# Optimization experiments

Hardware: AMD Instinct MI355X
Metric: run time of the kernel (lower is better)

The kernel has to match this reference:

```python
import jax, jax.numpy as jnp
import numpy as np

K = 16
EPS = 1e-5
SLOPE = 0.01  # nn.LeakyReLU default


def _bn(x, g, b):
    # BatchNorm1d in training mode applied to [N, C, k] in torch == normalize
    # per-channel over (N, k) axes of [N, k, C] here. Biased variance (ddof=0).
    m = x.mean(axis=(0, 1))
    v = x.var(axis=(0, 1))
    return (x - m) * jax.lax.rsqrt(v + EPS) * g + b


def _lrelu(x):
    return jnp.where(x >= 0, x, SLOPE * x)


def setup_inputs() -> dict:
    key = jax.random.key(0)
    ks = jax.random.split(key, 24)
    N, CIN, COUT = 8192, 256, 256
    s = 0.05
    inp = {
        "fea_i": jax.random.normal(ks[0], (N, CIN), jnp.float32),
        "fea_last": jax.random.normal(ks[1], (N, CIN), jnp.float32),
        "xyz_i": jax.random.uniform(ks[2], (N, 3), jnp.float32),
        "xyz_last": jax.random.uniform(ks[3], (N, 3), jnp.float32),
        "t_i": jnp.float32(2.0),
        "t_last": jnp.float32(1.0),
        # lin_p: Linear(4,64) -> BN(64) -> LeakyReLU -> Linear(64,COUT)
        "wp1": jax.random.normal(ks[4], (4, 64), jnp.float32) * s,
        "bp1": jnp.zeros((64,), jnp.float32),
        "gp": jnp.ones((64,), jnp.float32),
        "bp": jnp.zeros((64,), jnp.float32),
        "wp2": jax.random.normal(ks[5], (64, COUT), jnp.float32) * s,
        "bp2": jnp.zeros((COUT,), jnp.float32),
        # lin_q / lin_k / lin_v
        "wq": jax.random.normal(ks[6], (CIN, COUT), jnp.float32) * s,
        "bq": jnp.zeros((COUT,), jnp.float32),
        "wk": jax.random.normal(ks[7], (CIN, COUT), jnp.float32) * s,
        "bk": jnp.zeros((COUT,), jnp.float32),
        "wv": jax.random.normal(ks[8], (CIN, COUT), jnp.float32) * s,
        "bv": jnp.zeros((COUT,), jnp.float32),
        # lin_w: BN -> LeakyReLU -> Linear(COUT,COUT) -> BN -> LeakyReLU
        "gw1": jnp.ones((COUT,), jnp.float32),
        "bw1": jnp.zeros((COUT,), jnp.float32),
        "ww": jax.random.normal(ks[9], (COUT, COUT), jnp.float32) * s,
        "bw": jnp.zeros((COUT,), jnp.float32),
        "gw2": jnp.ones((COUT,), jnp.float32),
        "bw2": jnp.zeros((COUT,), jnp.float32),
    }
    return inp


def reference(fea_i, fea_last, xyz_i, xyz_last, t_i, t_last,
              wp1, bp1, gp, bp, wp2, bp2,
              wq, bq, wk, bk, wv, bv,
              gw1, bw1, ww, bw, gw2, bw2):
    # k-NN: for each query point in xyz_last, K nearest points in xyz_i
    d2 = (jnp.sum(xyz_last * xyz_last, -1)[:, None]
          + jnp.sum(xyz_i * xyz_i, -1)[None, :]
          - 2.0 * xyz_last @ xyz_i.T)              # [N, N]
    idx = jax.lax.top_k(-d2, K)[1]                 # [N, K] neighbor idx into xyz_i

    fi = fea_i[idx]                                # [N, K, CIN]
    xi = xyz_i[idx]                                # [N, K, 3]
    # pe = xyzt_i - xyzt_last ; the gathered "last" side is the query point itself
    pe = jnp.concatenate([xi - xyz_last[:, None, :],
                          (t_i - t_last) * jnp.ones_like(xi[..., :1])], axis=-1)  # [N,K,4]
    pe = pe @ wp1 + bp1
    pe = _lrelu(_bn(pe, gp, bp))
    pe = pe @ wp2 + bp2                            # [N, K, COUT]

    q = fea_last @ wq + bq                         # [N, COUT], broadcast over K
    w = q[:, None, :] - (fi @ wk + bk) + pe        # [N, K, COUT]
    w = _lrelu(_bn(w, gw1, bw1))
    w = w @ ww + bw
    w = _lrelu(_bn(w, gw2, bw2))
    w = jax.nn.softmax(w, axis=1)                  # softmax over K neighbors

    v = fi @ wv + bv + pe                          # [N, K, COUT]
    return jnp.sum(w * v, axis=1)                  # [N, COUT]
```

## Files before the change

kernel.cpp:

```cpp
#include <hip/hip_runtime.h>
#include <hip/hip_bf16.h>
#include <math.h>

#define N     8192
#define KNN   16
#define NK    (N*KNN)
#define C     256
#define CH    64
#define EPS   1e-5f
#define SLOPE 0.01f
#define LISTMAX 512

typedef __hip_bfloat16 bf16;
typedef short bfrag __attribute__((ext_vector_type(8)));
typedef float ffrag __attribute__((ext_vector_type(4)));

__device__ __forceinline__ float b2f(bf16 x){ return __bfloat162float(x); }
__device__ __forceinline__ bf16  f2b(float x){ return __float2bfloat16(x); }
__device__ __forceinline__ float b2fu(unsigned short s){
    return __uint_as_float(((unsigned)s) << 16);
}
__device__ __forceinline__ unsigned short f2bu(float x){
    union { bf16 h; unsigned short s; } u; u.h = f2b(x); return u.s;
}

union BF8 { unsigned short s[8]; uint4 u; };

template<typename T> __device__ __forceinline__ float ldv(const void* p, int i);
template<> __device__ __forceinline__ float ldv<float>(const void* p, int i){
    return ((const float*)p)[i];
}
template<> __device__ __forceinline__ float ldv<bf16>(const void* p, int i){
    return __bfloat162float(((const bf16*)p)[i]);
}
__device__ __forceinline__ bool is_f32(const void* ti){
    return ((const unsigned short*)ti)[0] == 0;
}

template<typename T>
__device__ __forceinline__ void stage8(const void* src, size_t off,
                                       unsigned short* dst){
    if (sizeof(T) == 4){
        const float4* s = (const float4*)((const float*)src + off);
        float4 a = s[0], b = s[1];
        BF8 o;
        o.s[0]=f2bu(a.x); o.s[1]=f2bu(a.y); o.s[2]=f2bu(a.z); o.s[3]=f2bu(a.w);
        o.s[4]=f2bu(b.x); o.s[5]=f2bu(b.y); o.s[6]=f2bu(b.z); o.s[7]=f2bu(b.w);
        *(uint4*)dst = o.u;
    } else {
        *(uint4*)dst = *(const uint4*)((const unsigned short*)src + off);
    }
}

__device__ __forceinline__ int mbcnt64(unsigned long long b){
    return __builtin_amdgcn_mbcnt_hi((unsigned)(b>>32),
           __builtin_amdgcn_mbcnt_lo((unsigned)b, 0));
}
__device__ __forceinline__ unsigned d2key(float d2){
    unsigned u = __float_as_uint(d2);
    return u ^ (((unsigned)(((int)u) >> 31)) | 0x80000000u);
}

__device__ __align__(256) int    g_idx[NK];
__device__ __align__(256) float  g_S[4096];
__device__ __align__(256) float  g_Rep[4*64*256];
__device__ __align__(256) float  g_M2[2048*9];
__device__ __align__(256) float4 g_pts[N];
__device__ __align__(256) int    g_cellCnt[4096];
__device__ __align__(256) int    g_cellStart[4100];
__device__ __align__(256) int    g_cellCur[4096];
__device__ __align__(256) float4 g_spts[N];
__device__ __align__(256) int    g_sidx[N];
__device__ __align__(256) unsigned short g_qT [C*C];
__device__ __align__(256) unsigned short g_kT [C*C];
__device__ __align__(256) unsigned short g_vT [C*C];
__device__ __align__(256) unsigned short g_wwT[C*C];
__device__ __align__(256) unsigned short g_p2T[C*CH];
__device__ __align__(256) unsigned short g_q  [N*C];
__device__ __align__(256) unsigned short g_fkb[N*C];
__device__ __align__(256) unsigned short g_fvb[N*C];
__device__ __align__(256) bf16   g_w1[NK*C];
__device__ __align__(256) bf16   g_vv[NK*C];
__device__ __align__(256) bf16   g_w2[NK*C];

__device__ __forceinline__ int cell_of(float4 c){
    int cx = (int)(c.x*16.f); cx = cx<0?0:(cx>15?15:cx);
    int cy = (int)(c.y*16.f); cy = cy<0?0:(cy>15?15:cy);
    int cz = (int)(c.z*16.f); cz = cz<0?0:(cz>15?15:cz);
    return (cz<<8) | (cy<<4) | cx;
}

__global__ __launch_bounds__(256) void kprepall(const void* xyz_i,
        const void* wq, const void* wk, const void* wv, const void* ww,
        const void* wp2, const void* ti_){
#pragma clang fp contract(off)
    const int b = blockIdx.x, tid = threadIdx.x;
    const bool f = is_f32(ti_);
    if (b < 64){
        int i = b*256 + tid;
        #pragma unroll
        for (int k = 0; k < 4; k++) g_Rep[i*4 + k] = 0.f;
        if (b < 16) g_S[i] = 0.f;
        else if (b < 32) g_cellCnt[(b-16)*256 + tid] = 0;
    } else if (b < 96){
        int p = (b-64)*256 + tid;
        float x = f ? ldv<float>(xyz_i, p*3+0) : ldv<bf16>(xyz_i, p*3+0);
        float y = f ? ldv<float>(xyz_i, p*3+1) : ldv<bf16>(xyz_i, p*3+1);
        float z = f ? ldv<float>(xyz_i, p*3+2) : ldv<bf16>(xyz_i, p*3+2);
        g_pts[p] = make_float4(x, y, z, (x*x + y*y) + z*z);
    } else {
        const void* src; unsigned short* dst; int K; int i0;
        if      (b <  352){ src=wq;  dst=g_qT;  K=256; i0=(b-  96)*256; }
        else if (b <  608){ src=wk;  dst=g_kT;  K=256; i0=(b- 352)*256; }
        else if (b <  864){ src=wv;  dst=g_vT;  K=256; i0=(b- 608)*256; }
        else if (b < 1120){ src=ww;  dst=g_wwT; K=256; i0=(b- 864)*256; }
        else              { src=wp2; dst=g_p2T; K=64;  i0=(b-1120)*256; }
        int i = i0 + tid;
        int k = i >> 8, n = i & 255;
        float v = f ? ldv<float>(src, i) : ldv<bf16>(src, i);
        dst[n*K + k] = f2bu(v);
    }
}

__global__ __launch_bounds__(256) void khist(){
    int p = blockIdx.x*256 + threadIdx.x;
    atomicAdd(&g_cellCnt[cell_of(g_pts[p])], 1);
}
__global__ __launch_bounds__(256) void kscan(){
    __shared__ int sc[256];
    const int tid = threadIdx.x;
    int carry = 0;
    for (int ch = 0; ch < 16; ch++){
        int i = ch*256 + tid;
        int v = g_cellCnt[i];
        sc[tid] = v;
        __syncthreads();
        for (int s = 1; s < 256; s <<= 1){
            int t_ = (tid >= s) ? sc[tid - s] : 0;
            __syncthreads();
            sc[tid] += t_;
            __syncthreads();
        }
        int excl = carry + sc[tid] - v;
        g_cellStart[i] = excl;
        g_cellCur[i]   = excl;
        carry += sc[255];
        __syncthreads();
    }
    if (tid == 0) g_cellStart[4096] = carry;
}
__global__ __launch_bounds__(256) void kscatter(){
    int p = blockIdx.x*256 + threadIdx.x;
    float4 c = g_pts[p];
    int pos = atomicAdd(&g_cellCur[cell_of(c)], 1);
    g_spts[pos] = c;
    g_sidx[pos] = p;
}

template<int D>
__device__ unsigned sel16(float qx, float qy, float qz, float sq, int lane){
#pragma clang fp contract(off)
    unsigned kk[D];
    #pragma unroll
    for (int i = 0; i < D; i++) kk[i] = 0xFFFFFFFFu;
    for (int t = 0; t < N/64; t++){
        float4 c = g_pts[t*64 + lane];
        float dot = (qx*c.x + qy*c.y) + qz*c.z;
        float d2  = (sq + c.w) - 2.0f*dot;
        unsigned u = d2key(d2);
        #pragma unroll
        for (int j = D-1; j > 0; --j){
            unsigned hi = (kk[j-1] > u) ? kk[j-1] : u;
            kk[j] = (kk[j] < hi) ? kk[j] : hi;
        }
        kk[0] = (kk[0] < u) ? kk[0] : u;
    }
    unsigned v16 = 0;
    for (int it = 0; it < 16; ++it){
        unsigned m = kk[0];
        #pragma unroll
        for (int s = 1; s < 64; s <<= 1){
            unsigned o = (unsigned)__shfl_xor((int)m, s, 64);
            m = (m < o) ? m : o;
        }
        unsigned long long ball = __ballot(kk[0] == m);
        int w = __ffsll(ball) - 1;
        if (lane == w){
            #pragma unroll
            for (int j = 0; j < D-1; j++) kk[j] = kk[j+1];
            kk[D-1] = 0xFFFFFFFFu;
        }
        v16 = m;
    }
    return v16;
}

__device__ int2 scan16(float qx, float qy, float qz, float sq, unsigned v16,
                       int lane, int* sure, int* tie){
#pragma clang fp contract(off)
    int nsure = 0, ntie = 0;
    for (int t = 0; t < N/64; t++){
        const int p = t*64 + lane;
        float4 c = g_pts[p];
        float dot = (qx*c.x + qy*c.y) + qz*c.z;
        float d2  = (sq + c.w) - 2.0f*dot;
        unsigned u = d2key(d2);
        bool bs = (u < v16), bt = (u == v16);
        unsigned long long Bs = __ballot(bs);
        unsigned long long Bt = __ballot(bt);
        if (bs){
            int pos = nsure + mbcnt64(Bs);
            if (pos < 16) sure[pos] = p;
        }
        if (bt){
            int pos = ntie + mbcnt64(Bt);
            if (pos < 16) tie[pos] = p;
        }
        nsure += (int)__popcll(Bs);
        ntie  += (int)__popcll(Bt);
    }
    return make_int2(nsure, ntie);
}

template<typename T>
__device__ void kknn_body(const void* xyz_last, int* sureL, int* tieL,
                          int* listL, float* momL){
#pragma clang fp contract(off)
    const int lane  = threadIdx.x & 63;
    const int wslot = threadIdx.x >> 6;
    const int q     = (blockIdx.x*256 + threadIdx.x) >> 6;
    const float qx = ldv<T>(xyz_last, q*3+0);
    const float qy = ldv<T>(xyz_last, q*3+1);
    const float qz = ldv<T>(xyz_last, q*3+2);
    const float sq = (qx*qx + qy*qy) + qz*qz;
    int* sure = &sureL[wslot*16];
    int* tie  = &tieL [wslot*16];
    int* list = &listL[wslot*LISTMAX];

    int cqx = (int)(qx*16.f); cqx = cqx<0?0:(cqx>15?15:cqx);
    int cqy = (int)(qy*16.f); cqy = cqy<0?0:(cqy>15?15:cqy);
    int cqz = (int)(qz*16.f); cqz = cqz<0?0:(cqz>15?15:cqz);

    int cnt0 = 0, cnt1 = 0, cs0 = 0, cs1 = 0;
    #pragma unroll
    for (int h = 0; h < 2; h++){
        int idx = lane*2 + h;
        if (idx < 125){
            int iz = idx/25, r = idx - iz*25, iy = r/5, ix = r - iy*5;
            int cx = cqx+ix-2, cy = cqy+iy-2, cz = cqz+iz-2;
            if ((unsigned)cx < 16u && (unsigned)cy < 16u && (unsigned)cz < 16u){
                int cell = (cz<<8) | (cy<<4) | cx;
                int s = g_cellStart[cell], e = g_cellStart[cell+1];
                if (h == 0){ cs0 = s; cnt0 = e - s; }
                else       { cs1 = s; cnt1 = e - s; }
            }
        }
    }
    int tot = cnt0 + cnt1;
    int incl = tot;
    #pragma unroll
    for (int s = 1; s < 64; s <<= 1){
        int u = __shfl_up(incl, s, 64);
        if (lane >= s) incl += u;
    }
    const int Tn = __shfl(incl, 63, 64);
    int base = incl - tot;
    bool full = (Tn > LISTMAX) || (Tn < 16);
    unsigned v16 = 0;
    int nsure = 0, ntie = 0;
    if (!full){
        for (int i = 0; i < cnt0; i++) list[base+i] = cs0 + i;
        for (int i = 0; i < cnt1; i++) list[base+cnt0+i] = cs1 + i;
        unsigned kk[4] = {~0u,~0u,~0u,~0u};
        int chunks = (Tn + 63) >> 6;
        for (int t = 0; t < chunks; t++){
            int li = t*64 + lane;
            unsigned u = 0xFFFFFFFFu;
            if (li < Tn){
                float4 c = g_spts[list[li]];
                float dot = (qx*c.x + qy*c.y) + qz*c.z;
                u = d2key((sq + c.w) - 2.0f*dot);
            }
            #pragma unroll
            for (int j = 3; j > 0; --j){
                unsigned hi = (kk[j-1] > u) ? kk[j-1] : u;
                kk[j] = (kk[j] < hi) ? kk[j] : hi;
            }
            kk[0] = (kk[0] < u) ? kk[0] : u;
        }
        for (int it = 0; it < 16; ++it){
            unsigned m = kk[0];
            #pragma unroll
            for (int s = 1; s < 64; s <<= 1){
                unsigned o = (unsigned)__shfl_xor((int)m, s, 64);
                m = (m < o) ? m : o;
            }
            unsigned long long ball = __ballot(kk[0] == m);
            int w = __ffsll(ball) - 1;
            if (lane == w){
                kk[0]=kk[1]; kk[1]=kk[2]; kk[2]=kk[3]; kk[3]=0xFFFFFFFFu;
            }
            v16 = m;
        }
        const float h_ = 0.0625f;
        float dmin = 1e30f;
        if (cqx-2 > 0)  dmin = fminf(dmin, qx - (float)(cqx-2)*h_);
        if (cqx+3 < 16) dmin = fminf(dmin, (float)(cqx+3)*h_ - qx);
        if (cqy-2 > 0)  dmin = fminf(dmin, qy - (float)(cqy-2)*h_);
        if (cqy+3 < 16) dmin = fminf(dmin, (float)(cqy+3)*h_ - qy);
        if (cqz-2 > 0)  dmin = fminf(dmin, qz - (float)(cqz-2)*h_);
        if (cqz+3 < 16) dmin = fminf(dmin, (float)(cqz+3)*h_ - qz);
        unsigned ub = d2key(dmin*dmin);
        if (!(v16 < ub)) full = true;
    }
    if (!full){
        int chunks = (Tn + 63) >> 6;
        for (int t = 0; t < chunks; t++){
            int li = t*64 + lane;
            unsigned u = 0xFFFFFFFFu; int oi = 0;
            if (li < Tn){
                int pos = list[li];
                float4 c = g_spts[pos];
                oi = g_sidx[pos];
                float dot = (qx*c.x + qy*c.y) + qz*c.z;
                u = d2key((sq + c.w) - 2.0f*dot);
            }
            bool bs = (li < Tn) && (u < v16);
            bool bt = (li < Tn) && (u == v16);
            unsigned long long Bs = __ballot(bs);
            unsigned long long Bt = __ballot(bt);
            if (bs){
                int pos2 = nsure + mbcnt64(Bs);
                if (pos2 < 16) sure[pos2] = oi;
            }
            if (bt){
                int pos2 = ntie + mbcnt64(Bt);
                if (pos2 < 16) tie[pos2] = oi;
            }
            nsure += (int)__popcll(Bs);
            ntie  += (int)__popcll(Bt);
        }
        if (nsure > 16 || (ntie > 16 && nsure < 16)) full = true;
    }
    const bool gridok = !full;
    if (full){
        v16 = sel16<16>(qx, qy, qz, sq, lane);
        int2 c2 = scan16(qx, qy, qz, sq, v16, lane, sure, tie);
        nsure = c2.x; ntie = c2.y;
    }
    if (nsure > 16) nsure = 16;
    int vsel = 0;
    if (lane < 16 && lane < nsure) vsel = sure[lane];
    if (gridok){
        int tv = (lane < (ntie < 16 ? ntie : 16)) ? tie[lane] : 0x7FFFFFFF;
        #pragma unroll
        for (int k = 2; k <= 16; k <<= 1)
            #pragma unroll
            for (int j = k>>1; j > 0; j >>= 1){
                int o = __shfl_xor(tv, j, 64);
                bool asc = ((lane & k) == 0);
                bool low = ((lane & j) == 0);
                int mn = tv < o ? tv : o;
                int mx = tv < o ? o : tv;
                tv = (asc == low) ? mn : mx;
            }
        int tfrom = __shfl(tv, (lane - nsure) & 63, 64);
        if (lane < 16 && lane >= nsure) vsel = tfrom;
    } else {
        if (lane < 16 && lane >= nsure) vsel = tie[lane - nsure];
    }
    float dx = 0.f, dy = 0.f, dz = 0.f;
    if (lane < 16){
        if ((unsigned)vsel >= (unsigned)N) vsel = 0;
        g_idx[q*KNN + lane] = vsel;
        float4 c = g_pts[vsel];
        dx = c.x - qx; dy = c.y - qy; dz = c.z - qz;
    }
    float mm[9] = {dx, dy, dz, dx*dx, dx*dy, dx*dz, dy*dy, dy*dz, dz*dz};
    #pragma unroll
    for (int j = 0; j < 9; j++){
        #pragma unroll
        for (int s = 1; s < 16; s <<= 1)
            mm[j] += __shfl_xor(mm[j], s, 64);
    }
    if (lane == 0){
        #pragma unroll
        for (int j = 0; j < 9; j++) momL[wslot*9 + j] = mm[j];
    }
    __syncthreads();
    if (threadIdx.x < 9){
        int t = threadIdx.x;
        g_M2[blockIdx.x*9 + t] = momL[t] + momL[9+t] + momL[18+t] + momL[27+t];
    }
}
__global__ __launch_bounds__(256) void kknn(const void* xyz_last, const void* ti_){
    __shared__ int sureL[4*16];
    __shared__ int tieL [4*16];
    __shared__ int listL[4*LISTMAX];
    __shared__ float momL[4*9];
    if (is_f32(ti_)) kknn_body<float>(xyz_last, sureL, tieL, listL, momL);
    else             kknn_body<bf16 >(xyz_last, sureL, tieL, listL, momL);
}

template<typename T>
__device__ void kgemm3m_body(const void* A, const unsigned short* BT,
                             const void* bias, unsigned short* out,
                             unsigned short* Al, unsigned short* Bl){
    const int tid  = threadIdx.x;
    const int c0   = blockIdx.x*128, r0 = blockIdx.y*128;
    const int lane = tid & 63, wv = tid >> 6;
    const int m    = lane & 15, qd = lane >> 4;
    const int rw   = (wv >> 1)*64, cw = (wv & 1)*64;
    ffrag acc[4][4];
    #pragma unroll
    for (int i = 0; i < 4; i++)
        #pragma unroll
        for (int j = 0; j < 4; j++)
            #pragma unroll
            for (int r = 0; r < 4; r++) acc[i][j][r] = 0.f;
    const int arow = tid >> 2, ach = tid & 3;
    for (int kt = 0; kt < 8; ++kt){
        __syncthreads();
        #pragma unroll
        for (int p = 0; p < 2; ++p){
            int row = arow + p*64;
            stage8<T>(A, (size_t)(r0+row)*C + kt*32 + ach*8, &Al[row*40 + ach*8]);
            *(uint4*)&Bl[row*40 + ach*8] =
                *(const uint4*)&BT[(c0+row)*C + kt*32 + ach*8];
        }
        __syncthreads();
        bfrag af[4], bfr[4];
        #pragma unroll
        for (int i = 0; i < 4; i++)
            af[i] = *(const bfrag*)&Al[(rw + i*16 + m)*40 + qd*8];
        #pragma unroll
        for (int j = 0; j < 4; j++)
            bfr[j] = *(const bfrag*)&Bl[(cw + j*16 + m)*40 + qd*8];
        #pragma unroll
        for (int i = 0; i < 4; i++)
            #pragma unroll
            for (int j = 0; j < 4; j++)
                acc[i][j] = __builtin_amdgcn_mfma_f32_16x16x32_bf16(
                                af[i], bfr[j], acc[i][j], 0, 0, 0);
    }
    float b4[4];
    #pragma unroll
    for (int j = 0; j < 4; j++) b4[j] = ldv<T>(bias, c0 + cw + j*16 + m);
    #pragma unroll
    for (int i = 0; i < 4; i++){
        #pragma unroll
        for (int r = 0; r < 4; r++){
            int row = r0 + rw + i*16 + qd*4 + r;
            unsigned short* orow = &out[(size_t)row*C];
            #pragma unroll
            for (int j = 0; j < 4; j++)
                orow[c0 + cw + j*16 + m] = f2bu(acc[i][j][r] + b4[j]);
        }
    }
}
__global__ __launch_bounds__(256) void kgemm3m(const void* fea_i, const void* fea_last,
        const void* bq, const void* bk, const void* bv, const void* ti_){
    __shared__ unsigned short Al[128*40];
    __shared__ unsigned short Bl[128*40];
    const int which = blockIdx.z;
    const void* A = (which==0) ? fea_last : fea_i;
    const unsigned short* BT = (which==0) ? g_qT : (which==1) ? g_kT : g_vT;
    const void* bias = (which==0) ? bq : (which==1) ? bk : bv;
    unsigned short* out = (which==0) ? g_q : (which==1) ? g_fkb : g_fvb;
    if (is_f32(ti_)) kgemm3m_body<float>(A, BT, bias, out, Al, Bl);
    else             kgemm3m_body<bf16 >(A, BT, bias, out, Al, Bl);
}

template<typename T>
__device__ void kfinpe_body(const void* wp1, const void* bp1,
                            const void* gp, const void* bp_,
                            const void* t_i, const void* t_last,
                            float* mTot, float* wred){
    const int tid = threadIdx.x, lane = tid & 63, wv = tid >> 6;
    float p[9];
    #pragma unroll
    for (int j = 0; j < 9; j++) p[j] = 0.f;
    for (int i = tid; i < 2048; i += 256){
        const float* m = &g_M2[i*9];
        #pragma unroll
        for (int j = 0; j < 9; j++) p[j] += m[j];
    }
    #pragma unroll
    for (int j = 0; j < 9; j++){
        #pragma unroll
        for (int s = 1; s < 64; s <<= 1) p[j] += __shfl_xor(p[j], s, 64);
    }
    if (lane == 0){
        #pragma unroll
        for (int j = 0; j < 9; j++) wred[wv*9 + j] = p[j];
    }
    __syncthreads();
    if (tid < 9) mTot[tid] = wred[tid] + wred[9+tid] + wred[18+tid] + wred[27+tid];
    __syncthreads();
    if (tid >= 64) return;
    const int c = tid;
    float M[9];
    #pragma unroll
    for (int j = 0; j < 9; j++) M[j] = mTot[j];
    const float w0 = ldv<T>(wp1, c),     w1 = ldv<T>(wp1, 64+c);
    const float w2 = ldv<T>(wp1, 128+c), w3 = ldv<T>(wp1, 192+c);
    const float dt = ldv<T>(t_i, 0) - ldv<T>(t_last, 0);
    const float be = dt*w3 + ldv<T>(bp1, c);
    const float NKf = (float)NK;
    float lin  = w0*M[0] + w1*M[1] + w2*M[2];
    float quad = w0*w0*M[3] + w1*w1*M[6] + w2*w2*M[8]
               + 2.f*(w0*w1*M[4] + w0*w2*M[5] + w1*w2*M[7]);
    float mean = (lin + NKf*be) / NKf;
    float ev2  = (quad + 2.f*be*lin + NKf*be*be) / NKf;
    float var  = ev2 - mean*mean;
    float sc   = ldv<T>(gp, c) * rsqrtf(var + EPS);
    g_S[128+c] = sc;
    g_S[192+c] = ldv<T>(bp_, c) - mean*sc;
}
__global__ void kfinpe(const void* wp1, const void* bp1, const void* gp,
                       const void* bp_, const void* t_i, const void* t_last){
    __shared__ float mTot[9];
    __shared__ float wred[4*9];
    if (is_f32(t_i)) kfinpe_body<float>(wp1, bp1, gp, bp_, t_i, t_last, mTot, wred);
    else             kfinpe_body<bf16 >(wp1, bp1, gp, bp_, t_i, t_last, mTot, wred);
}

__global__ void kfinalize(int Cn, int outOff, const void* g, const void* b,
                          const void* ti_, int repA){
    int c = threadIdx.x;
    if (c >= Cn) return;
    float s = 0.f, ss = 0.f;
    for (int r = 0; r < 64; r++){
        s  += g_Rep[((repA  )*64 + r)*256 + c];
        ss += g_Rep[((repA+1)*64 + r)*256 + c];
    }
    bool f = is_f32(ti_);
    float mean = s / (float)NK;
    float var  = ss / (float)NK - mean*mean;
    float gv = f ? ldv<float>(g, c) : ldv<bf16>(g, c);
    float bv = f ? ldv<float>(b, c) : ldv<bf16>(b, c);
    float sc = gv * rsqrtf(var + EPS);
    g_S[outOff+c]    = sc;
    g_S[outOff+Cn+c] = bv - mean*sc;
}

template<typename T>
__device__ void kpe2m_body(const void* xyz_i, const void* xyz_last,
                           const void* wp1, const void* bp1, const void* bp2,
                           const void* t_i, const void* t_last,
                           unsigned short* Apel, unsigned short* Bpl, int* gl,
                           float* s1w, float* s2w){
    const int tid  = threadIdx.x;
    const int lane = tid & 63, wv = tid >> 6;
    const int m    = lane & 15, qd = lane >> 4;
    const int rw   = (wv >> 1)*64, cw = (wv & 1)*64;
    const int c0   = blockIdx.x*128, r0 = blockIdx.y*128;
    if (tid < 128) gl[tid] = g_idx[r0 + tid];
    { int row = tid >> 1, half = tid & 1;
      #pragma unroll
      for (int e = 0; e < 4; e++)
          *(uint4*)&Bpl[row*72 + half*32 + e*8] =
              *(const uint4*)&g_p2T[(c0+row)*CH + half*32 + e*8];
    }
    __syncthreads();
    { const int kp = lane;
      const float w0 = ldv<T>(wp1, kp),     w1 = ldv<T>(wp1, 64+kp);
      const float w2 = ldv<T>(wp1, 128+kp), w3 = ldv<T>(wp1, 192+kp);
      const float b0 = ldv<T>(bp1, kp);
      const float sc = g_S[128+kp], sh = g_S[128+64+kp];
      const float dt = ldv<T>(t_i, 0) - ldv<T>(t_last, 0);
      #pragma unroll 4
      for (int p = 0; p < 32; p++){
          int row = wv*32 + p;
          int R = r0 + row; int n = R >> 4; int g = gl[row];
          float dx = ldv<T>(xyz_i, g*3+0) - ldv<T>(xyz_last, n*3+0);
          float dy = ldv<T>(xyz_i, g*3+1) - ldv<T>(xyz_last, n*3+1);
          float dz = ldv<T>(xyz_i, g*3+2) - ldv<T>(xyz_last, n*3+2);
          float v = dx*w0 + dy*w1 + dz*w2 + dt*w3 + b0;
          v = v*sc + sh;
          v = (v >= 0.f) ? v : SLOPE*v;
          Apel[row*72 + kp] = f2bu(v);
      } }
    __syncthreads();
    ffrag acc[4][4];
    #pragma unroll
    for (int i = 0; i < 4; i++)
        #pragma unroll
        for (int j = 0; j < 4; j++)
            #pragma unroll
            for (int r = 0; r < 4; r++) acc[i][j][r] = 0.f;
    #pragma unroll
    for (int ks = 0; ks < 2; ++ks){
        bfrag af[4], bfr[4];
        #pragma unroll
        for (int i = 0; i < 4; i++)
            af[i] = *(const bfrag*)&Apel[(rw + i*16 + m)*72 + ks*32 + qd*8];
        #pragma unroll
        for (int j = 0; j < 4; j++)
            bfr[j] = *(const bfrag*)&Bpl[(cw + j*16 + m)*72 + ks*32 + qd*8];
        #pragma unroll
        for (int i = 0; i < 4; i++)
            #pragma unroll
            for (int j = 0; j < 4; j++)
                acc[i][j] = __builtin_amdgcn_mfma_f32_16x16x32_bf16(
                                af[i], bfr[j], acc[i][j], 0, 0, 0);
    }
    float bp2v[4];
    #pragma unroll
    for (int j = 0; j < 4; j++) bp2v[j] = ldv<T>(bp2, c0 + cw + j*16 + m);
    float cs[4] = {0.f,0.f,0.f,0.f}, cq[4] = {0.f,0.f,0.f,0.f};
    #pragma unroll
    for (int i = 0; i < 4; i++){
        #pragma unroll
        for (int r = 0; r < 4; r++){
            int row = rw + i*16 + qd*4 + r;
            int R = r0 + row; int n = R >> 4; int g = gl[row];
            const unsigned short* qr  = &g_q  [(size_t)n*C];
            const unsigned short* fkr = &g_fkb[(size_t)g*C];
            const unsigned short* fvr = &g_fvb[(size_t)g*C];
            #pragma unroll
            for (int j = 0; j < 4; j++){
                int col = c0 + cw + j*16 + m;
                float pe = acc[i][j][r] + bp2v[j];
                unsigned short bb = f2bu(b2fu(qr[col]) - b2fu(fkr[col]) + pe);
                ((unsigned short*)g_w1)[(size_t)R*C + col] = bb;
                float rv = b2fu(bb);
                cs[j] += rv; cq[j] += rv*rv;
                ((unsigned short*)g_vv)[(size_t)R*C + col] =
                    f2bu(b2fu(fvr[col]) + pe);
            }
        }
    }
    #pragma unroll
    for (int j = 0; j < 4; j++){
        cs[j] += __shfl_xor(cs[j], 16, 64); cs[j] += __shfl_xor(cs[j], 32, 64);
        cq[j] += __shfl_xor(cq[j], 16, 64); cq[j] += __shfl_xor(cq[j], 32, 64);
    }
    if (lane < 16){
        #pragma unroll
        for (int j = 0; j < 4; j++){
            s1w[(wv>>1)*128 + cw + j*16 + lane] = cs[j];
            s2w[(wv>>1)*128 + cw + j*16 + lane] = cq[j];
        }
    }
    __syncthreads();
    if (tid < 128){
        float a = s1w[tid] + s1w[128+tid];
        float b = s2w[tid] + s2w[128+tid];
        int rep = blockIdx.y & 63;
        atomicAdd(&g_Rep[(0*64 + rep)*256 + c0 + tid], a);
        atomicAdd(&g_Rep[(1*64 + rep)*256 + c0 + tid], b);
    }
}
__global__ __launch_bounds__(256) void kpe2m(const void* xyz_i, const void* xyz_last,
        const void* wp1, const void* bp1, const void* bp2,
        const void* t_i, const void* t_last){
    __shared__ unsigned short Apel[128*72];
    __shared__ unsigned short Bpl[128*72];
    __shared__ int gl[128];
    __shared__ float s1w[256], s2w[256];
    if (is_f32(t_i))
        kpe2m_body<float>(xyz_i, xyz_last, wp1, bp1, bp2, t_i, t_last,
                          Apel, Bpl, gl, s1w, s2w);
    else
        kpe2m_body<bf16 >(xyz_i, xyz_last, wp1, bp1, bp2, t_i, t_last,
                          Apel, Bpl, gl, s1w, s2w);
}

template<typename T>
__device__ void kgemmww_body(const void* bw, unsigned short* Al,
                             unsigned short* Bl, float* scl, float* shl,
                             float* t1w, float* t2w){
    const int tid  = threadIdx.x;
    const int c0   = blockIdx.x*128, r0 = blockIdx.y*128;
    const int lane = tid & 63, wv = tid >> 6;
    const int m    = lane & 15, qd = lane >> 4;
    const int rw   = (wv >> 1)*64, cw = (wv & 1)*64;
    scl[tid] = g_S[768 + tid]; shl[tid] = g_S[768 + C + tid];
    ffrag acc[4][4];
    #pragma unroll
    for (int i = 0; i < 4; i++)
        #pragma unroll
        for (int j = 0; j < 4; j++)
            #pragma unroll
            for (int r = 0; r < 4; r++) acc[i][j][r] = 0.f;
    const int arow = tid >> 2, ach = tid & 3;
    for (int kt = 0; kt < 8; ++kt){
        __syncthreads();
        #pragma unroll
        for (int p = 0; p < 2; ++p){
            int row = arow + p*64;
            int kk  = kt*32 + ach*8;
            BF8 in, o;
            in.u = *(const uint4*)&g_w1[(size_t)(r0+row)*C + kk];
            #pragma unroll
            for (int e = 0; e < 8; e++){
                float x = b2fu(in.s[e]);
                x = x*scl[kk+e] + shl[kk+e];
                x = (x >= 0.f) ? x : SLOPE*x;
                o.s[e] = f2bu(x);
            }
            *(uint4*)&Al[row*40 + ach*8] = o.u;
            *(uint4*)&Bl[row*40 + ach*8] =
                *(const uint4*)&g_wwT[(c0+row)*C + kt*32 + ach*8];
        }
        __syncthreads();
        bfrag af[4], bf_[4];
        #pragma unroll
        for (int i = 0; i < 4; i++)
            af[i] = *(const bfrag*)&Al[(rw + i*16 + m)*40 + qd*8];
        #pragma unroll
        for (int j = 0; j < 4; j++)
            bf_[j] = *(const bfrag*)&Bl[(cw + j*16 + m)*40 + qd*8];
        #pragma unroll
        for (int i = 0; i < 4; i++)
            #pragma unroll
            for (int j = 0; j < 4; j++)
                acc[i][j] = __builtin_amdgcn_mfma_f32_16x16x32_bf16(
                                af[i], bf_[j], acc[i][j], 0, 0, 0);
    }
    float bwv[4];
    #pragma unroll
    for (int j = 0; j < 4; j++) bwv[j] = ldv<T>(bw, c0 + cw + j*16 + m);
    float cs[4] = {0.f,0.f,0.f,0.f}, cq[4] = {0.f,0.f,0.f,0.f};
    #pragma unroll
    for (int j = 0; j < 4; j++){
        int col = c0 + cw + j*16 + m;
        #pragma unroll
        for (int i = 0; i < 4; i++){
            #pragma unroll
            for (int r = 0; r < 4; r++){
                int row = r0 + rw + i*16 + qd*4 + r;
                unsigned short bb = f2bu(acc[i][j][r] + bwv[j]);
                ((unsigned short*)g_w2)[(size_t)row*C + col] = bb;
                float rv = b2fu(bb);
                cs[j] += rv; cq[j] += rv*rv;
            }
        }
    }
    #pragma unroll
    for (int j = 0; j < 4; j++){
        cs[j] += __shfl_xor(cs[j], 16, 64); cs[j] += __shfl_xor(cs[j], 32, 64);
        cq[j] += __shfl_xor(cq[j], 16, 64); cq[j] += __shfl_xor(cq[j], 32, 64);
    }
    if (lane < 16){
        #pragma unroll
        for (int j = 0; j < 4; j++){
            t1w[(wv>>1)*128 + cw + j*16 + lane] = cs[j];
            t2w[(wv>>1)*128 + cw + j*16 + lane] = cq[j];
        }
    }
    __syncthreads();
    if (tid < 128){
        float a = t1w[tid] + t1w[128+tid];
        float b = t2w[tid] + t2w[128+tid];
        int rep = blockIdx.y & 63;
        atomicAdd(&g_Rep[(2*64 + rep)*256 + c0 + tid], a);
        atomicAdd(&g_Rep[(3*64 + rep)*256 + c0 + tid], b);
    }
}
__global__ __launch_bounds__(256) void kgemmww(const void* bw, const void* ti_){
    __shared__ unsigned short Al[128*40];
    __shared__ unsigned short Bl[128*40];
    __shared__ float scl[C], shl[C];
    __shared__ float t1w[256], t2w[256];
    if (is_f32(ti_)) kgemmww_body<float>(bw, Al, Bl, scl, shl, t1w, t2w);
    else             kgemmww_body<bf16 >(bw, Al, Bl, scl, shl, t1w, t2w);
}

__global__ __launch_bounds__(256) void kfinal(void* out, const void* ti_){
    const int n = blockIdx.x, c = threadIdx.x;
    const float sc = g_S[1792+c], sh = g_S[1792+C+c];
    float u[KNN];
    float m = -3.4e38f;
    #pragma unroll
    for (int k = 0; k < KNN; k++){
        float x = b2f(g_w2[(size_t)(n*KNN+k)*C + c])*sc + sh;
        x = (x >= 0.f) ? x : SLOPE*x;
        u[k] = x; m = fmaxf(m, x);
    }
    float ssum = 0.f, o = 0.f;
    #pragma unroll
    for (int k = 0; k < KNN; k++){
        float e = __expf(u[k] - m);
        ssum += e;
        o += e * b2f(g_vv[(size_t)(n*KNN+k)*C + c]);
    }
    float r = o / ssum;
    if (is_f32(ti_)) ((float*)out)[(size_t)n*C + c] = r;
    else             ((bf16*)out)[(size_t)n*C + c] = f2b(r);
}

extern "C" void kernel_launch(void* const* d_in, const int* in_sizes, int n_in,
                              void* d_out, int out_size, void* d_ws, size_t ws_size,
                              hipStream_t stream){
    const void* fea_i    = d_in[0];
    const void* fea_last = d_in[1];
    const void* xyz_i    = d_in[2];
    const void* xyz_last = d_in[3];
    const void* t_i      = d_in[4];
    const void* t_last   = d_in[5];
    const void* wp1 = d_in[6];
    const void* bp1 = d_in[7];
    const void* gp  = d_in[8];
    const void* bp_ = d_in[9];
    const void* wp2 = d_in[10];
    const void* bp2 = d_in[11];
    const void* wq  = d_in[12];
    const void* bq  = d_in[13];
    const void* wk  = d_in[14];
    const void* bk  = d_in[15];
    const void* wv  = d_in[16];
    const void* bv  = d_in[17];
    const void* gw1 = d_in[18];
    const void* bw1 = d_in[19];
    const void* ww  = d_in[20];
    const void* bw  = d_in[21];
    const void* gw2 = d_in[22];
    const void* bw2 = d_in[23];

    kprepall<<<1184, 256, 0, stream>>>(xyz_i, wq, wk, wv, ww, wp2, t_i);
    khist<<<32, 256, 0, stream>>>();
    kscan<<<1, 256, 0, stream>>>();
    kscatter<<<32, 256, 0, stream>>>();
    kknn<<<N/4, 256, 0, stream>>>(xyz_last, t_i);
    kgemm3m<<<dim3(2, 64, 3), 256, 0, stream>>>(fea_i, fea_last, bq, bk, bv, t_i);
    kfinpe<<<1, 256, 0, stream>>>(wp1, bp1, gp, bp_, t_i, t_last);
    kpe2m<<<dim3(2, NK/128), 256, 0, stream>>>(xyz_i, xyz_last, wp1, bp1, bp2,
                                               t_i, t_last);
    kfinalize<<<1, 256, 0, stream>>>(256, 768, gw1, bw1, t_i, 0);
    kgemmww<<<dim3(2, NK/128), 256, 0, stream>>>(bw, t_i);
    kfinalize<<<1, 256, 0, stream>>>(256, 1792, gw2, bw2, t_i, 2);
    kfinal<<<N, 256, 0, stream>>>(d_out, t_i);
}
```

Before: 322.1 us.

## Stage PE epilogue through LDS for 16-byte vectorized global loads and stores

The kpe2m epilogue now writes the MFMA accumulator tile (with bias added) into shared memory that aliases the A/B staging buffers, one 64-column half at a time. It then re-reads it in a row-major layout so each thread handles 8 contiguous columns. This lets the q/fk/fv gathers and the w1/vv writes use 16-byte vector accesses instead of scattered 2-byte accesses. In exchange it adds extra barriers, an LDS round trip, and a longer shuffle reduction for the BN statistics, with two atomic passes per block.

```diff
diff --git a/kernel.cpp b/kernel.cpp
--- a/kernel.cpp
+++ b/kernel.cpp
@@ -544,12 +544,13 @@
     g_S[outOff+Cn+c] = bv - mean*sc;
 }
 
+#define PE_LDP 68
 template<typename T>
 __device__ void kpe2m_body(const void* xyz_i, const void* xyz_last,
                            const void* wp1, const void* bp1, const void* bp2,
                            const void* t_i, const void* t_last,
-                           unsigned short* Apel, unsigned short* Bpl, int* gl,
-                           float* s1w, float* s2w){
+                           unsigned short* Apel, unsigned short* Bpl,
+                           float* peL, int* gl, float* s1w, float* s2w){
     const int tid  = threadIdx.x;
     const int lane = tid & 63, wv = tid >> 6;
     const int m    = lane & 15, qd = lane >> 4;
@@ -608,63 +609,96 @@
     float bp2v[4];
     #pragma unroll
     for (int j = 0; j < 4; j++) bp2v[j] = ldv<T>(bp2, c0 + cw + j*16 + m);
-    float cs[4] = {0.f,0.f,0.f,0.f}, cq[4] = {0.f,0.f,0.f,0.f};
-    #pragma unroll
-    for (int i = 0; i < 4; i++){
-        #pragma unroll
-        for (int r = 0; r < 4; r++){
-            int row = rw + i*16 + qd*4 + r;
+    #pragma unroll
+    for (int i = 0; i < 4; i++)
+        #pragma unroll
+        for (int j = 0; j < 4; j++)
+            #pragma unroll
+            for (int r = 0; r < 4; r++) acc[i][j][r] += bp2v[j];
+
+    const int rep = blockIdx.y & 63;
+    const int cg  = tid & 7;
+    const int rg  = tid >> 3;
+    for (int h = 0; h < 2; ++h){
+        __syncthreads();
+        if ((wv & 1) == h){
+            #pragma unroll
+            for (int i = 0; i < 4; i++)
+                #pragma unroll
+                for (int j = 0; j < 4; j++)
+                    #pragma unroll
+                    for (int r = 0; r < 4; r++)
+                        peL[(rw + i*16 + qd*4 + r)*PE_LDP + j*16 + m]
+                            = acc[i][j][r];
+        }
+        __syncthreads();
+        float cs8[8], cq8[8];
+        #pragma unroll
+        for (int e = 0; e < 8; e++){ cs8[e] = 0.f; cq8[e] = 0.f; }
+        #pragma unroll
+        for (int rr = 0; rr < 4; rr++){
+            int row = rg*4 + rr;
             int R = r0 + row; int n = R >> 4; int g = gl[row];
-            const unsigned short* qr  = &g_q  [(size_t)n*C];
-            const unsigned short* fkr = &g_fkb[(size_t)g*C];
-            const unsigned short* fvr = &g_fvb[(size_t)g*C];
-            #pragma unroll
-            for (int j = 0; j < 4; j++){
-                int col = c0 + cw + j*16 + m;
-                float pe = acc[i][j][r] + bp2v[j];
-                unsigned short bb = f2bu(b2fu(qr[col]) - b2fu(fkr[col]) + pe);
-                ((unsigned short*)g_w1)[(size_t)R*C + col] = bb;
+            int colb = c0 + h*64 + cg*8;
+            BF8 qb, kb, vb;
+            qb.u = *(const uint4*)&g_q  [(size_t)n*C + colb];
+            kb.u = *(const uint4*)&g_fkb[(size_t)g*C + colb];
+            vb.u = *(const uint4*)&g_fvb[(size_t)g*C + colb];
+            float4 p0 = *(const float4*)&peL[row*PE_LDP + cg*8];
+            float4 p1 = *(const float4*)&peL[row*PE_LDP + cg*8 + 4];
+            float pe8[8] = {p0.x,p0.y,p0.z,p0.w,p1.x,p1.y,p1.z,p1.w};
+            BF8 w1o, vvo;
+            #pragma unroll
+            for (int e = 0; e < 8; e++){
+                float pv = pe8[e];
+                unsigned short bb = f2bu(b2fu(qb.s[e]) - b2fu(kb.s[e]) + pv);
+                w1o.s[e] = bb;
                 float rv = b2fu(bb);
-                cs[j] += rv; cq[j] += rv*rv;
-                ((unsigned short*)g_vv)[(size_t)R*C + col] =
-                    f2bu(b2fu(fvr[col]) + pe);
-            }
-        }
-    }
-    #pragma unroll
-    for (int j = 0; j < 4; j++){
-        cs[j] += __shfl_xor(cs[j], 16, 64); cs[j] += __shfl_xor(cs[j], 32, 64);
-        cq[j] += __shfl_xor(cq[j], 16, 64); cq[j] += __shfl_xor(cq[j], 32, 64);
-    }
-    if (lane < 16){
-        #pragma unroll
-        for (int j = 0; j < 4; j++){
-            s1w[(wv>>1)*128 + cw + j*16 + lane] = cs[j];
-            s2w[(wv>>1)*128 + cw + j*16 + lane] = cq[j];
-        }
-    }
-    __syncthreads();
-    if (tid < 128){
-        float a = s1w[tid] + s1w[128+tid];
-        float b = s2w[tid] + s2w[128+tid];
-        int rep = blockIdx.y & 63;
-        atomicAdd(&g_Rep[(0*64 + rep)*256 + c0 + tid], a);
-        atomicAdd(&g_Rep[(1*64 + rep)*256 + c0 + tid], b);
+                cs8[e] += rv; cq8[e] += rv*rv;
+                vvo.s[e] = f2bu(b2fu(vb.s[e]) + pv);
+            }
+            *(uint4*)&((unsigned short*)g_w1)[(size_t)R*C + colb] = w1o.u;
+            *(uint4*)&((unsigned short*)g_vv)[(size_t)R*C + colb] = vvo.u;
+        }
+        #pragma unroll
+        for (int e = 0; e < 8; e++){
+            #pragma unroll
+            for (int s_ = 8; s_ < 64; s_ <<= 1){
+                cs8[e] += __shfl_xor(cs8[e], s_, 64);
+                cq8[e] += __shfl_xor(cq8[e], s_, 64);
+            }
+        }
+        if (lane < 8){
+            #pragma unroll
+            for (int e = 0; e < 8; e++){
+                s1w[wv*64 + lane*8 + e] = cs8[e];
+                s2w[wv*64 + lane*8 + e] = cq8[e];
+            }
+        }
+        __syncthreads();
+        if (tid < 64){
+            float a = s1w[tid] + s1w[64+tid] + s1w[128+tid] + s1w[192+tid];
+            float b = s2w[tid] + s2w[64+tid] + s2w[128+tid] + s2w[192+tid];
+            atomicAdd(&g_Rep[(0*64 + rep)*256 + c0 + h*64 + tid], a);
+            atomicAdd(&g_Rep[(1*64 + rep)*256 + c0 + h*64 + tid], b);
+        }
     }
 }
 __global__ __launch_bounds__(256) void kpe2m(const void* xyz_i, const void* xyz_last,
         const void* wp1, const void* bp1, const void* bp2,
         const void* t_i, const void* t_last){
-    __shared__ unsigned short Apel[128*72];
-    __shared__ unsigned short Bpl[128*72];
+    __shared__ __align__(16) unsigned char smem[128*72*2*2];
     __shared__ int gl[128];
     __shared__ float s1w[256], s2w[256];
+    unsigned short* Apel = (unsigned short*)smem;
+    unsigned short* Bpl  = Apel + 128*72;
+    float* peL = (float*)smem;
     if (is_f32(t_i))
         kpe2m_body<float>(xyz_i, xyz_last, wp1, bp1, bp2, t_i, t_last,
-                          Apel, Bpl, gl, s1w, s2w);
+                          Apel, Bpl, peL, gl, s1w, s2w);
     else
         kpe2m_body<bf16 >(xyz_i, xyz_last, wp1, bp1, bp2, t_i, t_last,
-                          Apel, Bpl, gl, s1w, s2w);
+                          Apel, Bpl, peL, gl, s1w, s2w);
 }
 
 template<typename T>
```

Measured after the change: 313.1 us. -2.8%, faster.
